# Kernel optimization log

Hardware: AMD Instinct MI355X
Metric: run time of the kernel (lower is better)

The kernel has to match this reference:

```python
import jax, jax.numpy as jnp
import numpy as np
from jax import lax

K = 8  # diffusion channels
T = 3  # diffusion steps


def setup_inputs() -> dict:
    key = jax.random.key(0)
    k1, k2, k3 = jax.random.split(key, 3)
    x = jax.random.normal(k1, (16, 1, 512, 512), dtype=jnp.float32)
    # per-step conv weights [T, out=k, in=1, kh, kw] and biases [T, k]
    W = jax.random.normal(k2, (T, K, 1, 3, 3), dtype=jnp.float32) * 0.1
    b = jax.random.normal(k3, (T, K), dtype=jnp.float32) * 0.1
    return {"x": x, "W": W, "b": b}


def _g(d):
    # mode 1 edge-stopping function: exp(-|d| / (1 + d^2))
    return jnp.exp(-jnp.abs(d) / (1.0 + d * d))


def reference(x, W, b):
    in_x = x  # [N,1,H,W]
    for t in range(T):
        d1 = lax.conv_general_dilated(
            in_x, W[t], window_strides=(1, 1), padding="SAME",
            dimension_numbers=("NCHW", "OIHW", "NCHW"),
        ) + b[t][None, :, None, None]  # [N,K,H,W]
        features = _g(d1) * d1
        # squash_tensor: sum over the K channels, keep channel dim of 1
        in_x = in_x - jnp.sum(features, axis=1, keepdims=True) / K
    return in_x
```

## Files before the change

kernel.cpp:

```cpp
#include <hip/hip_runtime.h>

static constexpr int IMG = 512;
static constexpr int TX  = 64;
static constexpr int TY  = 32;
static constexpr int LST = 72;
static constexpr int SROWS = TY + 6;

template<int WOFF, int NR, int RLO, int NG, bool TO_GLOBAL>
__device__ __forceinline__ void diffuse_step(
    const float* __restrict__ prev, float* __restrict__ cur,
    const float* __restrict__ Wt, const float* __restrict__ bt,
    int xoff , int ty0, int tx0,
    int tid, float* __restrict__ gout)
{
    constexpr int LOADW  = WOFF ? 8 : 6;
    constexpr int NITEMS = NR * NG;
    for (int idx = tid; idx < NITEMS; idx += 256) {
        const int rr = idx / NG;
        const int j  = idx - rr * NG;
        const int r  = RLO + rr;
        const int c0 = 4 * j;
        const float* base = prev + (r - 1) * LST + c0;

        float L0[LOADW], L1[LOADW], L2[LOADW];
        *(float4*)&L0[0] = *(const float4*)(base);
        *(float4*)&L1[0] = *(const float4*)(base + LST);
        *(float4*)&L2[0] = *(const float4*)(base + 2 * LST);
        if (WOFF) {
            *(float4*)&L0[4] = *(const float4*)(base + 4);
            *(float4*)&L1[4] = *(const float4*)(base + LST + 4);
            *(float4*)&L2[4] = *(const float4*)(base + 2 * LST + 4);
        } else {
            *(float2*)&L0[4] = *(const float2*)(base + 4);
            *(float2*)&L1[4] = *(const float2*)(base + LST + 4);
            *(float2*)&L2[4] = *(const float2*)(base + 2 * LST + 4);
        }

        float acc[4] = {0.f, 0.f, 0.f, 0.f};
#pragma unroll
        for (int k = 0; k < 8; ++k) {
            const float w0 = Wt[9*k+0], w1 = Wt[9*k+1], w2 = Wt[9*k+2];
            const float w3 = Wt[9*k+3], w4 = Wt[9*k+4], w5 = Wt[9*k+5];
            const float w6 = Wt[9*k+6], w7 = Wt[9*k+7], w8 = Wt[9*k+8];
            const float bk = bt[k];
#pragma unroll
            for (int i = 0; i < 4; ++i) {
                float d = bk;
                d = fmaf(w0, L0[WOFF+i],   d);
                d = fmaf(w1, L0[WOFF+i+1], d);
                d = fmaf(w2, L0[WOFF+i+2], d);
                d = fmaf(w3, L1[WOFF+i],   d);
                d = fmaf(w4, L1[WOFF+i+1], d);
                d = fmaf(w5, L1[WOFF+i+2], d);
                d = fmaf(w6, L2[WOFF+i],   d);
                d = fmaf(w7, L2[WOFF+i+1], d);
                d = fmaf(w8, L2[WOFF+i+2], d);
                const float t    = fmaf(d, d, 1.0f);
                const float rinv = __builtin_amdgcn_rcpf(t);
                const float e    = __builtin_amdgcn_exp2f(
                                       -1.442695040888963f * __builtin_fabsf(d) * rinv);
                acc[i] = fmaf(e, d, acc[i]);
            }
        }

        float4 v;
        v.x = L1[WOFF+1] - acc[0] * 0.125f;
        v.y = L1[WOFF+2] - acc[1] * 0.125f;
        v.z = L1[WOFF+3] - acc[2] * 0.125f;
        v.w = L1[WOFF+4] - acc[3] * 0.125f;

        const int gy = ty0 - 3 + r;
        if (TO_GLOBAL) {
            *(float4*)&gout[gy * IMG + tx0 + c0] = v;
        } else {
            const bool ry  = (unsigned)gy < (unsigned)IMG;
            const int  gx0 = xoff + c0;
            v.x = (ry && (unsigned)(gx0 + 0) < (unsigned)IMG) ? v.x : 0.f;
            v.y = (ry && (unsigned)(gx0 + 1) < (unsigned)IMG) ? v.y : 0.f;
            v.z = (ry && (unsigned)(gx0 + 2) < (unsigned)IMG) ? v.z : 0.f;
            v.w = (ry && (unsigned)(gx0 + 3) < (unsigned)IMG) ? v.w : 0.f;
            *(float4*)&cur[r * LST + c0] = v;
        }
    }
}

__global__ __launch_bounds__(256, 6) void deep_ad_kernel(
    const float* __restrict__ x, const float* __restrict__ W,
    const float* __restrict__ b, float* __restrict__ out)
{
    __shared__ float A[SROWS * LST];
    __shared__ float Bs[SROWS * LST];

    const int tid = threadIdx.x;
    const int tx0 = blockIdx.x * TX;
    const int ty0 = blockIdx.y * TY;
    const float* xin  = x   + (size_t)blockIdx.z * (IMG * IMG);
    float*       gout = out + (size_t)blockIdx.z * (IMG * IMG);

    for (int idx = tid; idx < SROWS * 18; idx += 256) {
        const int r = idx / 18, j = idx - (idx / 18) * 18;
        const int gy = ty0 - 3 + r;
        const int gx = tx0 - 4 + 4 * j;
        float4 v = {0.f, 0.f, 0.f, 0.f};
        if ((unsigned)gy < (unsigned)IMG && (unsigned)gx < (unsigned)IMG)
            v = *(const float4*)(xin + gy * IMG + gx);
        *(float4*)&A[r * LST + 4 * j] = v;
    }
    __syncthreads();

    diffuse_step<1, TY + 4, 1, 17, false>(A,  Bs, W + 0,   b + 0,  tx0 - 2, ty0, tx0, tid, nullptr);
    __syncthreads();
    diffuse_step<0, TY + 2, 2, 17, false>(Bs, A,  W + 72,  b + 8,  tx0 - 1, ty0, tx0, tid, nullptr);
    __syncthreads();
    diffuse_step<0, TY,     3, 16, true >(A, nullptr, W + 144, b + 16, 0, ty0, tx0, tid, gout);
}

extern "C" void kernel_launch(void* const* d_in, const int* in_sizes, int n_in,
                              void* d_out, int out_size, void* d_ws, size_t ws_size,
                              hipStream_t stream)
{
    const float* x = (const float*)d_in[0];
    const float* W = (const float*)d_in[1];
    const float* b = (const float*)d_in[2];
    float* out = (float*)d_out;
    const int N = in_sizes[0] / (IMG * IMG);
    dim3 grid(IMG / TX, IMG / TY, N);
    deep_ad_kernel<<<grid, 256, 0, stream>>>(x, W, b, out);
}
```

Before: 130.7 us.

## Use single-wavefront blocks with smaller tiles and software-prefetched LDS loads

Shrinks the tile height from 32 to 16 rows and launches 64-thread blocks, one wavefront each, instead of 256 threads. Each step loop now prefetches the next item's 3x3 stencil window from shared memory while computing the current one. The global staging load is batched into registers before being written to LDS. This aims to hide LDS latency and reduce barrier cost, but it raises the halo recompute ratio (6 extra rows per 16 instead of per 32) and removes the occupancy hint from the launch bounds.

```diff
diff --git a/kernel.cpp b/kernel.cpp
--- a/kernel.cpp
+++ b/kernel.cpp
@@ -2,27 +2,25 @@
 
 static constexpr int IMG = 512;
 static constexpr int TX  = 64;
-static constexpr int TY  = 32;
+static constexpr int TY  = 16;
 static constexpr int LST = 72;
-static constexpr int SROWS = TY + 6;
+static constexpr int SROWS  = TY + 6;
+static constexpr int NSTAGE = SROWS * 18;
 
 template<int WOFF, int NR, int RLO, int NG, bool TO_GLOBAL>
 __device__ __forceinline__ void diffuse_step(
     const float* __restrict__ prev, float* __restrict__ cur,
     const float* __restrict__ Wt, const float* __restrict__ bt,
-    int xoff , int ty0, int tx0,
-    int tid, float* __restrict__ gout)
+    int xoff, int ty0, int tx0, int tid, float* __restrict__ gout)
 {
     constexpr int LOADW  = WOFF ? 8 : 6;
     constexpr int NITEMS = NR * NG;
-    for (int idx = tid; idx < NITEMS; idx += 256) {
-        const int rr = idx / NG;
-        const int j  = idx - rr * NG;
-        const int r  = RLO + rr;
-        const int c0 = 4 * j;
-        const float* base = prev + (r - 1) * LST + c0;
 
-        float L0[LOADW], L1[LOADW], L2[LOADW];
+    float L0[LOADW], L1[LOADW], L2[LOADW];
+    {
+        const int idx0 = (tid < NITEMS) ? tid : 0;
+        const int rr = idx0 / NG, j = idx0 - rr * NG;
+        const float* base = prev + (RLO + rr - 1) * LST + 4 * j;
         *(float4*)&L0[0] = *(const float4*)(base);
         *(float4*)&L1[0] = *(const float4*)(base + LST);
         *(float4*)&L2[0] = *(const float4*)(base + 2 * LST);
@@ -35,6 +33,30 @@
             *(float2*)&L1[4] = *(const float2*)(base + LST + 4);
             *(float2*)&L2[4] = *(const float2*)(base + 2 * LST + 4);
         }
+    }
+
+    for (int idx = tid; idx < NITEMS; idx += 64) {
+        float P0[LOADW], P1[LOADW], P2[LOADW];
+        {
+            const int nidx = (idx + 64 < NITEMS) ? (idx + 64) : idx;
+            const int rr = nidx / NG, j = nidx - rr * NG;
+            const float* base = prev + (RLO + rr - 1) * LST + 4 * j;
+            *(float4*)&P0[0] = *(const float4*)(base);
+            *(float4*)&P1[0] = *(const float4*)(base + LST);
+            *(float4*)&P2[0] = *(const float4*)(base + 2 * LST);
+            if (WOFF) {
+                *(float4*)&P0[4] = *(const float4*)(base + 4);
+                *(float4*)&P1[4] = *(const float4*)(base + LST + 4);
+                *(float4*)&P2[4] = *(const float4*)(base + 2 * LST + 4);
+            } else {
+                *(float2*)&P0[4] = *(const float2*)(base + 4);
+                *(float2*)&P1[4] = *(const float2*)(base + LST + 4);
+                *(float2*)&P2[4] = *(const float2*)(base + 2 * LST + 4);
+            }
+        }
+
+        const int rr = idx / NG, j = idx - rr * NG;
+        const int r  = RLO + rr, c0 = 4 * j;
 
         float acc[4] = {0.f, 0.f, 0.f, 0.f};
 #pragma unroll
@@ -81,10 +103,13 @@
             v.w = (ry && (unsigned)(gx0 + 3) < (unsigned)IMG) ? v.w : 0.f;
             *(float4*)&cur[r * LST + c0] = v;
         }
+
+#pragma unroll
+        for (int q = 0; q < LOADW; ++q) { L0[q] = P0[q]; L1[q] = P1[q]; L2[q] = P2[q]; }
     }
 }
 
-__global__ __launch_bounds__(256, 6) void deep_ad_kernel(
+__global__ __launch_bounds__(64) void deep_ad_kernel(
     const float* __restrict__ x, const float* __restrict__ W,
     const float* __restrict__ b, float* __restrict__ out)
 {
@@ -97,14 +122,24 @@
     const float* xin  = x   + (size_t)blockIdx.z * (IMG * IMG);
     float*       gout = out + (size_t)blockIdx.z * (IMG * IMG);
 
-    for (int idx = tid; idx < SROWS * 18; idx += 256) {
-        const int r = idx / 18, j = idx - (idx / 18) * 18;
-        const int gy = ty0 - 3 + r;
-        const int gx = tx0 - 4 + 4 * j;
-        float4 v = {0.f, 0.f, 0.f, 0.f};
-        if ((unsigned)gy < (unsigned)IMG && (unsigned)gx < (unsigned)IMG)
-            v = *(const float4*)(xin + gy * IMG + gx);
-        *(float4*)&A[r * LST + 4 * j] = v;
+    {
+        float4 sv[7];
+#pragma unroll
+        for (int q = 0; q < 7; ++q) {
+            const int item = tid + 64 * q;
+            const int rr = item / 18, j = item - rr * 18;
+            const int gy = ty0 - 3 + rr;
+            const int gx = tx0 - 4 + 4 * j;
+            float4 v = {0.f, 0.f, 0.f, 0.f};
+            if (item < NSTAGE && (unsigned)gy < (unsigned)IMG && (unsigned)gx < (unsigned)IMG)
+                v = *(const float4*)(xin + gy * IMG + gx);
+            sv[q] = v;
+        }
+#pragma unroll
+        for (int q = 0; q < 7; ++q) {
+            const int item = tid + 64 * q;
+            if (item < NSTAGE) *(float4*)&A[item * 4] = sv[q];
+        }
     }
     __syncthreads();
 
@@ -125,5 +160,5 @@
     float* out = (float*)d_out;
     const int N = in_sizes[0] / (IMG * IMG);
     dim3 grid(IMG / TX, IMG / TY, N);
-    deep_ad_kernel<<<grid, 256, 0, stream>>>(x, W, b, out);
+    deep_ad_kernel<<<grid, 64, 0, stream>>>(x, W, b, out);
 }
```

Measured after the change: 126.7 us. 1.03x faster.
